# Kernel tuning notes

Hardware: AMD Instinct MI355X
Metric: run time of the kernel (lower is better)

Reference implementation:

```python
import jax, jax.numpy as jnp
import numpy as np

L, M, DIN, DEM, DH, GH, DOUT = 4, 4, 128, 64, 400, 256, 8
B = 16384
EPS = 1e-5


def setup_inputs() -> dict:
    key = jax.random.key(0)
    ks = iter(jax.random.split(key, 48))
    def p(shape, s=0.05):
        return jax.random.normal(next(ks), shape, jnp.float32) * s
    return dict(
        x=p((B, DIN), 1.0), embedding_input=p((B, DEM), 1.0),
        base_w1=p((DIN, DH)), base_b1=p((DH,)), base_w2=p((DH, DH)), base_b2=p((DH,)),
        em_w=p((DEM, DH)), em_b=p((DH,)),
        gfc_w1=p((DH, GH)), gfc_b1=p((GH,)), gfc_w2=p((GH, GH)), gfc_b2=p((GH,)),
        gw0_w=p((GH, M * M)), gw0_b=p((M * M,)),
        cond1_w=p((M * M, GH)), cond1_b=p((GH,)), gw1_w=p((GH, M * M)), gw1_b=p((M * M,)),
        cond2_w=p((2 * M * M, GH)), cond2_b=p((GH,)), gw2_w=p((GH, M * M)), gw2_b=p((M * M,)),
        condL_w=p((3 * M * M, GH)), condL_b=p((GH,)), gwL_w=p((GH, M)), gwL_b=p((M,)),
        bn1_g=1.0 + p((L, M, DH)), bn1_b=p((L, M, DH)),
        mod_W=p((L, M, DH, DH)), mod_b=p((L, M, DH)),
        bn2_g=1.0 + p((L, M, DH)), bn2_b=p((L, M, DH)),
        last_w=p((DH, DOUT)), last_b=p((DOUT,)),
    )


def _bn(h, g, b):
    # training-mode BatchNorm1d over batch axis; h:[B,M,D], g,b:[M,D]
    mu = h.mean(axis=0)
    var = ((h - mu) ** 2).mean(axis=0)  # biased variance, as torch BN
    return (h - mu) / jnp.sqrt(var + EPS) * g + b


def reference(x, embedding_input,
              base_w1, base_b1, base_w2, base_b2, em_w, em_b,
              gfc_w1, gfc_b1, gfc_w2, gfc_b2,
              gw0_w, gw0_b, cond1_w, cond1_b, gw1_w, gw1_b,
              cond2_w, cond2_b, gw2_w, gw2_b,
              condL_w, condL_b, gwL_w, gwL_b,
              bn1_g, bn1_b, mod_W, mod_b, bn2_g, bn2_b,
              last_w, last_b):
    relu = jax.nn.relu
    b = x.shape[0]
    # base MLP (last activation = identity)
    out = relu(x @ base_w1 + base_b1) @ base_w2 + base_b2          # [B,DH]
    # embedding MLP (single layer, identity last activation)
    emb = embedding_input @ em_w + em_b                            # [B,DH]
    emb = emb * out                                                # cond_ob
    out = relu(out)
    # gating trunk
    emb = relu(emb)
    emb = relu(emb @ gfc_w1 + gfc_b1)
    emb = emb @ gfc_w2 + gfc_b2                                    # [B,GH]
    # routing weight 0
    raw0 = relu(emb) @ gw0_w + gw0_b                               # [B,M*M]
    w0 = jax.nn.softmax(raw0.reshape(b, M, M), axis=-1)
    weights = [w0]
    flat = [w0.reshape(b, M * M)]
    # cascaded routing weights (num_layers-2 = 2 extra)
    for cw, cb, gw, gb in ((cond1_w, cond1_b, gw1_w, gw1_b),
                           (cond2_w, cond2_b, gw2_w, gw2_b)):
        cond = jnp.concatenate(flat, axis=-1) @ cw + cb            # [B,GH]
        cond = relu(cond * emb)
        w = jax.nn.softmax((cond @ gw + gb).reshape(b, M, M), axis=-1)
        weights.append(w)
        flat.append(w.reshape(b, M * M))
    # last (per-module) gating weight
    cond = jnp.concatenate(flat, axis=-1) @ condL_w + condL_b
    cond = relu(cond * emb)
    last_weight = jax.nn.softmax(cond @ gwL_w + gwL_b, axis=-1)    # [B,M]
    # module layer 0: all modules see the same input
    h = jnp.broadcast_to(out[:, None, :], (b, M, DH))
    h = _bn(h, bn1_g[0], bn1_b[0])
    mo = jnp.einsum('bmi,mio->bmo', h, mod_W[0]) + mod_b[0]
    mo = _bn(mo, bn2_g[0], bn2_b[0])                               # [B,M,DH]
    # cascaded module layers with soft routing
    for i in range(1, L):
        mi = relu(jnp.einsum('bkd,bjk->bjd', mo, weights[i - 1]))  # dispatch/combine
        h = _bn(mi, bn1_g[i], bn1_b[i])
        mo = jnp.einsum('bmi,mio->bmo', h, mod_W[i]) + mod_b[i]
        mo = _bn(mo, bn2_g[i], bn2_b[i])
    out = relu(jnp.einsum('bmd,bm->bd', mo, last_weight))
    return out @ last_w + last_b
```

## Files before the change

kernel.cpp:

```cpp
#include <hip/hip_runtime.h>
#include <hip/hip_bf16.h>

typedef __bf16 bf16_t;
typedef __bf16 bf16x8 __attribute__((ext_vector_type(8)));
typedef __bf16 bf16x4 __attribute__((ext_vector_type(4)));
typedef float  f32x4  __attribute__((ext_vector_type(4)));

#define BN_   16384
#define DIN_  128
#define DEM_  64
#define DH_   400
#define DHP_  416
#define DHA_  512
#define GH_   256
#define MM_   4
#define EPS_  1e-5f
#define PCOLS 448
#define NCH   128
#define NCHMI 512

__global__ __launch_bounds__(256) void k_detect(const unsigned* __restrict__ w,
                                                int* __restrict__ flag)
{
  __shared__ int cnt[256];
  int c = 0;
  for (int i = 0; i < 16; ++i) {
    unsigned v = w[threadIdx.x * 16 + i];
    float lo = __uint_as_float((v & 0xffffu) << 16);
    if (!(fabsf(lo) < 1e4f)) ++c;
  }
  cnt[threadIdx.x] = c;
  __syncthreads();
  if (threadIdx.x == 0) {
    int t = 0;
    for (int i = 0; i < 256; ++i) t += cnt[i];
    flag[0] = (t > 64) ? 1 : 0;
  }
}

__global__ void k_mfmaprobe(int* __restrict__ layC)
{
  int l = threadIdx.x & 63;
  bf16x8 av, bv;
#pragma unroll
  for (int e = 0; e < 8; ++e) { av[e] = (bf16_t)0.f; bv[e] = (bf16_t)0.f; }
  if ((l >> 4) == 0) av[0] = (bf16_t)(float)(l & 15);
  if (l == 0)        bv[0] = (bf16_t)1.f;
  f32x4 acc = {0.f, 0.f, 0.f, 0.f};
  acc = __builtin_amdgcn_mfma_f32_16x16x32_bf16(av, bv, acc, 0, 0, 0);
  if (l == 1) layC[0] = (acc[0] > 0.5f) ? 1 : 0;
}

__global__ __launch_bounds__(256) void k_convert(
    const void* __restrict__ src, bf16_t* __restrict__ dst, int n,
    const int* __restrict__ flag)
{
  const int f = flag[0];
  for (int i = blockIdx.x * 256 + threadIdx.x; i < n; i += gridDim.x * 256)
    dst[i] = f ? (bf16_t)((const float*)src)[i] : ((const bf16_t*)src)[i];
}

struct SmallTab {
  const void* src[26];
  bf16_t*     dst[26];
  int         n[26];
};

__global__ __launch_bounds__(256) void k_convert_smalls(SmallTab tab, const int* __restrict__ flag)
{
  const int f = flag[0];
  const void* s = tab.src[blockIdx.x];
  bf16_t*     d = tab.dst[blockIdx.x];
  const int   n = tab.n[blockIdx.x];
  for (int i = threadIdx.x; i < n; i += 256)
    d[i] = f ? (bf16_t)((const float*)s)[i] : ((const bf16_t*)s)[i];
}

template<bool SCALED>
__global__ __launch_bounds__(256) void k_transT(
    const void* __restrict__ src, size_t srcOff, size_t srcStride,
    bf16_t* __restrict__ dst, size_t dstStride,
    int K, int N, int KP, int NPa,
    const float* __restrict__ scale, const int* __restrict__ flag)
{
  __shared__ float T[64][65];
  const int f = flag ? flag[0] : 0;
  const int z = blockIdx.z;
  const float*  sf = (const float*) src + srcOff + (size_t)z * srcStride;
  const bf16_t* sb = (const bf16_t*)src + srcOff + (size_t)z * srcStride;
  bf16_t* dp = dst + (size_t)z * dstStride;
  const int k0 = blockIdx.x * 64, n0 = blockIdx.y * 64;
  const int lr = threadIdx.x >> 6, ln = threadIdx.x & 63;
#pragma unroll
  for (int p = 0; p < 16; ++p) {
    int kl = p * 4 + lr;
    int k = k0 + kl, n = n0 + ln;
    float v = 0.f;
    if (k < K && n < N)
      v = f ? sf[(size_t)k * N + n] : (float)sb[(size_t)k * N + n];
    if (SCALED && k < K) v *= scale[z * DHP_ + k];
    T[kl][ln] = v;
  }
  __syncthreads();
#pragma unroll
  for (int p = 0; p < 16; ++p) {
    int nl = p * 4 + lr;
    int n = n0 + nl, k = k0 + ln;
    if (n < NPa && k < KP) dp[(size_t)n * KP + k] = (bf16_t)T[ln][nl];
  }
}

__device__ __forceinline__ void gload_lds16(const bf16_t* g, bf16_t* l) {
#if __has_builtin(__builtin_amdgcn_global_load_lds)
  __builtin_amdgcn_global_load_lds((const __attribute__((address_space(1))) void*)g,
                                   (__attribute__((address_space(3))) void*)l, 16, 0, 0);
#else
  *(bf16x8*)l = *(const bf16x8*)g;
#endif
}

__device__ __forceinline__ void stage128x32(const bf16_t* __restrict__ g, int ld,
                                            bf16_t* lds, int t) {
  const int c1 = t + 256;
  const int q0 = ((t  & 3) ^ ((t  >> 3) & 3)) * 8;
  const int q1 = ((c1 & 3) ^ ((c1 >> 3) & 3)) * 8;
  gload_lds16(g + (size_t)(t  >> 2) * ld + q0, lds + t  * 8);
  gload_lds16(g + (size_t)(c1 >> 2) * ld + q1, lds + c1 * 8);
}

__device__ __forceinline__ void acc_zero(f32x4 (&acc)[4][4]) {
  const f32x4 z = {0.f, 0.f, 0.f, 0.f};
#pragma unroll
  for (int i = 0; i < 4; ++i)
#pragma unroll
    for (int j = 0; j < 4; ++j) acc[i][j] = z;
}

template<int KS>
__device__ __forceinline__ void gemm_staged(
    const bf16_t* __restrict__ ga, int lda,
    const bf16_t* __restrict__ gb, int ldb,
    bf16_t* ldsA, bf16_t* ldsB,
    int wr, int wc, int rr, int qq, int t,
    f32x4 (&acc)[4][4])
{
  const int qs = (qq ^ ((rr >> 1) & 3)) * 8;
  stage128x32(ga, lda, ldsA, t);
  stage128x32(gb, ldb, ldsB, t);
  int cur = 0;
#pragma unroll 1
  for (int ks = 0; ks < KS; ++ks) {
    __syncthreads();
    if (ks + 1 < KS) {
      stage128x32(ga + (ks + 1) * 32, lda, ldsA + (cur ^ 1) * 4096, t);
      stage128x32(gb + (ks + 1) * 32, ldb, ldsB + (cur ^ 1) * 4096, t);
    }
    const bf16_t* la = ldsA + cur * 4096;
    const bf16_t* lb = ldsB + cur * 4096;
    bf16x8 av[4], bv[4];
#pragma unroll
    for (int i = 0; i < 4; ++i)
      av[i] = *reinterpret_cast<const bf16x8*>(la + (wr + i * 16 + rr) * 32 + qs);
#pragma unroll
    for (int i = 0; i < 4; ++i)
      bv[i] = *reinterpret_cast<const bf16x8*>(lb + (wc + i * 16 + rr) * 32 + qs);
#pragma unroll
    for (int i = 0; i < 4; ++i)
#pragma unroll
      for (int j = 0; j < 4; ++j)
        acc[i][j] = __builtin_amdgcn_mfma_f32_16x16x32_bf16(av[i], bv[j], acc[i][j], 0, 0, 0);
    __syncthreads();
    cur ^= 1;
  }
}

template<int KS, bool RELU, bool OUTF32>
__global__ __launch_bounds__(256, 4) void k_gemm_bias(
    const bf16_t* __restrict__ A, int lda,
    const bf16_t* __restrict__ Bt, int ldb,
    const bf16_t* __restrict__ bias, int nbias,
    void* __restrict__ outv, int ldo, int nout,
    const int* __restrict__ layC)
{
  __shared__ bf16_t sAB[4 * 4096];
  const int lay = layC[0];
  const int t = threadIdx.x;
  const int w = t >> 6, lane = t & 63;
  const int rr = lane & 15, qq = lane >> 4;
  const int wr = (w >> 1) * 64, wc = (w & 1) * 64;
  const int rowT = blockIdx.x * 128, colT = blockIdx.y * 128;
  f32x4 acc[4][4]; acc_zero(acc);
// ... 194 lines not shown
  const int row0 = rowT + wr, col0 = colT + wc;
  float bjv[4];
  bool cok[4];
#pragma unroll
  for (int j = 0; j < 4; ++j) {
    int c = col0 + j * 16 + rr;
    bjv[j] = bM[m * DHA_ + c];
    cok[j] = (c < DHP_);
  }
  float s[4] = {0.f, 0.f, 0.f, 0.f}, q[4] = {0.f, 0.f, 0.f, 0.f};
  if (lay == 0) {
#pragma unroll
    for (int j = 0; j < 4; ++j) {
      if (!cok[j]) continue;
#pragma unroll
      for (int i = 0; i < 4; ++i)
#pragma unroll
        for (int e = 0; e < 4; ++e) {
          float v = acc[i][j][e] + bjv[j];
          s[j] += v; q[j] += v * v;
        }
    }
    bf16_t* eld = sAB + w * 2304;
#pragma unroll
    for (int p = 0; p < 2; ++p) {
#pragma unroll
      for (int ii = 0; ii < 2; ++ii) {
        int i = p * 2 + ii;
#pragma unroll
        for (int j = 0; j < 4; ++j)
#pragma unroll
          for (int e = 0; e < 4; ++e)
            eld[(ii * 16 + qq * 4 + e) * 72 + j * 16 + rr] = (bf16_t)(acc[i][j][e] + bjv[j]);
      }
#pragma unroll
      for (int rb = 0; rb < 4; ++rb) {
        int rl = rb * 8 + (lane >> 3);
        int c8 = (lane & 7) * 8;
        bf16x8 vv = *reinterpret_cast<const bf16x8*>(eld + rl * 72 + c8);
        int row = row0 + p * 32 + rl;
        int col = colT + wc + c8;
        if (col < DHP_)
          *reinterpret_cast<bf16x8*>(mo + ((size_t)row * MM_ + m) * DHP_ + col) = vv;
      }
    }
  } else {
#pragma unroll
    for (int j = 0; j < 4; ++j) {
#pragma unroll
      for (int i = 0; i < 4; ++i) {
#pragma unroll
        for (int e = 0; e < 4; ++e) {
          int row = row0 + i * 16 + rr;
          int col = col0 + j * 16 + qq * 4 + e;
          if (col >= DHP_) continue;
          float v = acc[i][j][e] + bM[m * DHA_ + col];
          mo[((size_t)row * MM_ + m) * DHP_ + col] = (bf16_t)v;
        }
      }
    }
  }
#pragma unroll
  for (int j = 0; j < 4; ++j) {
    s[j] += __shfl_xor(s[j], 16); s[j] += __shfl_xor(s[j], 32);
    q[j] += __shfl_xor(q[j], 16); q[j] += __shfl_xor(q[j], 32);
  }
  if (lane < 16) {
#pragma unroll
    for (int j = 0; j < 4; ++j) {
      rs[w >> 1][(w & 1) * 64 + j * 16 + lane] = s[j];
      rq[w >> 1][(w & 1) * 64 + j * 16 + lane] = q[j];
    }
  }
  __syncthreads();
  if (lay == 0 && t < 128) {
    int col = blockIdx.y * 128 + t;
    if (col < PCOLS) {
      ps[((size_t)blockIdx.x * MM_ + m) * PCOLS + col] = rs[0][t] + rs[1][t];
      pq[((size_t)blockIdx.x * MM_ + m) * PCOLS + col] = rq[0][t] + rq[1][t];
    }
  }
}

__global__ __launch_bounds__(256) void k_stats(
    const bf16_t* __restrict__ src, int nm,
    float* __restrict__ ps, float* __restrict__ pq,
    const int* __restrict__ layC)
{
  if (layC[0] == 0) return;
  __shared__ float lsum[4 * 52 * 8], lsq[4 * 52 * 8];
  const int m = blockIdx.x, ch = blockIdx.y;
  const int sub = threadIdx.x >> 6, lane = threadIdx.x & 63;
  float s[8], q[8];
#pragma unroll
  for (int e = 0; e < 8; ++e) { s[e] = 0.f; q[e] = 0.f; }
  if (lane < 52) {
    for (int i = 0; i < 32; ++i) {
      int b = ch * 128 + sub + i * 4;
      bf16x8 v = *reinterpret_cast<const bf16x8*>(src + ((size_t)b * nm + m) * DHP_ + lane * 8);
#pragma unroll
      for (int e = 0; e < 8; ++e) {
        float f = (float)v[e];
        s[e] += f; q[e] += f * f;
      }
    }
#pragma unroll
    for (int e = 0; e < 8; ++e) {
      lsum[(sub * 52 + lane) * 8 + e] = s[e];
      lsq [(sub * 52 + lane) * 8 + e] = q[e];
    }
  }
  __syncthreads();
  for (int idx = threadIdx.x; idx < 416; idx += 256) {
    float S = lsum[idx] + lsum[416 + idx] + lsum[832 + idx] + lsum[1248 + idx];
    float Q = lsq [idx] + lsq [416 + idx] + lsq [832 + idx] + lsq [1248 + idx];
    ps[((size_t)ch * MM_ + m) * PCOLS + idx] = S;
    pq[((size_t)ch * MM_ + m) * PCOLS + idx] = Q;
  }
}

template<int NCHT>
__global__ __launch_bounds__(512) void k_bnprep2(
    const float* __restrict__ ps, const float* __restrict__ pq, int per_m,
    const bf16_t* __restrict__ g, const bf16_t* __restrict__ b,
    float* __restrict__ s_o, float* __restrict__ t_o)
{
  __shared__ float lS[8][64], lQ[8][64];
  const int m = blockIdx.x, cg = blockIdx.y;
  const int sub = threadIdx.x >> 6, lane = threadIdx.x & 63;
  const int k = cg * 64 + lane;
  const int mm = per_m ? m : 0;
  float S = 0.f, Q = 0.f;
#pragma unroll 8
  for (int ch = sub; ch < NCHT; ch += 8) {
    size_t idx = ((size_t)ch * MM_ + mm) * PCOLS + k;
    S += ps[idx];
    Q += pq[idx];
  }
  lS[sub][lane] = S; lQ[sub][lane] = Q;
  __syncthreads();
  if (sub == 0 && k < DHP_) {
    float St = 0.f, Qt = 0.f;
#pragma unroll
    for (int i = 0; i < 8; ++i) { St += lS[i][lane]; Qt += lQ[i][lane]; }
    float s = 0.f, t = 0.f;
    if (k < DH_) {
      float mean = St * (1.f / BN_);
      float var  = fmaxf(Qt * (1.f / BN_) - mean * mean, 0.f);
      float rstd = rsqrtf(var + EPS_);
      s = (float)g[m * DH_ + k] * rstd;
      t = (float)b[m * DH_ + k] - mean * s;
    }
    s_o[m * DHP_ + k] = s;
    t_o[m * DHP_ + k] = t;
  }
}

__global__ __launch_bounds__(256) void k_foldB(
    const void* __restrict__ modW, size_t off, const bf16_t* __restrict__ modb,
    const float* __restrict__ t1v, float* __restrict__ bM,
    const int* __restrict__ flag)
{
  __shared__ float ls[256];
  const int f = flag[0];
  const int m = blockIdx.x, ncg = blockIdx.y;
  const int t = threadIdx.x;
  const int n = ncg * 64 + (t & 63);
  const int ks = t >> 6;
  float a = 0.f;
  if (n < DH_) {
    for (int k = ks * 100; k < ks * 100 + 100; ++k) {
      size_t idx = off + ((size_t)m * DH_ + k) * DH_ + n;
      float wv = f ? ((const float*)modW)[idx] : (float)((const bf16_t*)modW)[idx];
      a += t1v[m * DHP_ + k] * wv;
    }
  }
  ls[t] = a;
  __syncthreads();
  if (t < 64) {
    int nn = ncg * 64 + t;
    float v = ls[t] + ls[t + 64] + ls[t + 128] + ls[t + 192];
    if (nn < DH_) v += (float)modb[m * DH_ + nn];
    else v = 0.f;
    bM[m * DHA_ + nn] = v;
  }
  if (ncg == 6 && t < 64) bM[m * DHA_ + 448 + t] = 0.f;
}

__global__ __launch_bounds__(256) void k_mix(
    const bf16_t* __restrict__ mo, const float* __restrict__ s2v, const float* __restrict__ t2v,
    const float* __restrict__ wbuf, int woff, bf16_t* __restrict__ mi,
    float* __restrict__ ps, float* __restrict__ pq)
{
  __shared__ float sB[4 * 416], qB[4 * 416];
  const int ch = blockIdx.x;
  const int wave = threadIdx.x >> 6, lane = threadIdx.x & 63;
  const int d0 = lane * 8;
  float sx[4][8], tx[4][8];
  float sAcc[4][8], qAcc[4][8];
#pragma unroll
  for (int j = 0; j < 4; ++j)
#pragma unroll
    for (int e = 0; e < 8; ++e) { sAcc[j][e] = 0.f; qAcc[j][e] = 0.f; }
  if (lane < 52) {
#pragma unroll
    for (int k = 0; k < 4; ++k)
#pragma unroll
      for (int e = 0; e < 8; ++e) {
        sx[k][e] = s2v[k * DHP_ + d0 + e];
        tx[k][e] = t2v[k * DHP_ + d0 + e];
      }
  }
#pragma unroll 1
  for (int i = 0; i < 8; ++i) {
    int b = ch * 32 + wave + i * 4;
    float wv = (lane < 16) ? wbuf[(size_t)b * 52 + woff + lane] : 0.f;
    if (lane < 52) {
      float x[4][8];
#pragma unroll
      for (int k = 0; k < 4; ++k) {
        bf16x8 v = *reinterpret_cast<const bf16x8*>(mo + ((size_t)b * MM_ + k) * DHP_ + d0);
#pragma unroll
        for (int e = 0; e < 8; ++e)
          x[k][e] = (float)v[e] * sx[k][e] + tx[k][e];
      }
#pragma unroll
      for (int j = 0; j < 4; ++j) {
        float w0 = __shfl(wv, j * 4 + 0), w1 = __shfl(wv, j * 4 + 1);
        float w2 = __shfl(wv, j * 4 + 2), w3 = __shfl(wv, j * 4 + 3);
        bf16x8 ov;
#pragma unroll
        for (int e = 0; e < 8; ++e) {
          float a = fmaxf(x[0][e] * w0 + x[1][e] * w1 + x[2][e] * w2 + x[3][e] * w3, 0.f);
          ov[e] = (bf16_t)a;
          float r = (float)ov[e];
          sAcc[j][e] += r; qAcc[j][e] += r * r;
        }
        *reinterpret_cast<bf16x8*>(mi + ((size_t)b * MM_ + j) * DHP_ + d0) = ov;
      }
    }
  }
#pragma unroll 1
  for (int w = 0; w < 4; ++w) {
    if (wave == w && lane < 52) {
#pragma unroll
      for (int j = 0; j < 4; ++j)
#pragma unroll
        for (int e = 0; e < 8; ++e) {
          int idx = j * 416 + d0 + e;
          if (w == 0) { sB[idx] = sAcc[j][e]; qB[idx] = qAcc[j][e]; }
          else        { sB[idx] += sAcc[j][e]; qB[idx] += qAcc[j][e]; }
        }
    }
    __syncthreads();
  }
  for (int idx = threadIdx.x; idx < 4 * 416; idx += 256) {
    int j = idx / 416, col = idx - j * 416;
    ps[((size_t)ch * MM_ + j) * PCOLS + col] = sB[idx];
    pq[((size_t)ch * MM_ + j) * PCOLS + col] = qB[idx];
  }
}

__global__ __launch_bounds__(256) void k_gate(
    const bf16_t* __restrict__ emb,
    const bf16_t* __restrict__ gw0t, const bf16_t* __restrict__ gw0_b,
    const bf16_t* __restrict__ c1_w,  const bf16_t* __restrict__ c1_b,
    const bf16_t* __restrict__ gw1t, const bf16_t* __restrict__ gw1_b,
    const bf16_t* __restrict__ c2_w,  const bf16_t* __restrict__ c2_b,
    const bf16_t* __restrict__ gw2t, const bf16_t* __restrict__ gw2_b,
    const bf16_t* __restrict__ cL_w,  const bf16_t* __restrict__ cL_b,
    const bf16_t* __restrict__ gwLt, const bf16_t* __restrict__ gwL_b,
    float* __restrict__ wbuf)
{
  __shared__ float VBA[4][272], VBB[4][272];
  __shared__ float FLA[4][64], FLB[4][64];
  const int wave = threadIdx.x >> 6, lane = threadIdx.x & 63;
  float* vbA = VBA[wave];
  float* vbB = VBB[wave];
  float* flA = FLA[wave];
  float* flB = FLB[wave];
  const int bA = blockIdx.x * 8 + wave * 2, bB = bA + 1;
  const int wrIdx = lane * 4 + (lane >> 4) * 4;

  float eA[4], eB[4];
  {
    bf16x4 evA = *reinterpret_cast<const bf16x4*>(emb + (size_t)bA * GH_ + lane * 4);
    bf16x4 evB = *reinterpret_cast<const bf16x4*>(emb + (size_t)bB * GH_ + lane * 4);
    f32x4 rA, rB;
#pragma unroll
    for (int e = 0; e < 4; ++e) {
      eA[e] = (float)evA[e]; rA[e] = fmaxf(eA[e], 0.f);
      eB[e] = (float)evB[e]; rB[e] = fmaxf(eB[e], 0.f);
    }
    *reinterpret_cast<f32x4*>(vbA + wrIdx) = rA;
    *reinterpret_cast<f32x4*>(vbB + wrIdx) = rB;
  }
  __builtin_amdgcn_wave_barrier();

  const int hh = lane >> 4, jj = lane & 15;

  auto softmax4 = [&](float a) -> float {
    float m1 = fmaxf(a, __shfl_xor(a, 1));
    float mx = fmaxf(m1, __shfl_xor(m1, 2));
    float ex = __expf(a - mx);
    float sx = ex + __shfl_xor(ex, 1);
    float sm = sx + __shfl_xor(sx, 2);
    return ex / sm;
  };

  auto gw_phase = [&](const bf16_t* Wt, const bf16_t* Bb, int foff) {
    float a0A = 0.f, a1A = 0.f, a0B = 0.f, a1B = 0.f;
#pragma unroll
    for (int cc = 0; cc < 8; ++cc) {
      int c8 = (cc + hh * 2) & 7;
      int k  = hh * 64 + c8 * 8;
      int idx = k + hh * 4;
      f32x4 vA0 = *reinterpret_cast<const f32x4*>(vbA + idx);
      f32x4 vA1 = *reinterpret_cast<const f32x4*>(vbA + idx + 4);
      f32x4 vB0 = *reinterpret_cast<const f32x4*>(vbB + idx);
      f32x4 vB1 = *reinterpret_cast<const f32x4*>(vbB + idx + 4);
      bf16x8 wv = *reinterpret_cast<const bf16x8*>(Wt + jj * 256 + k);
      float w0 = (float)wv[0], w1 = (float)wv[1], w2 = (float)wv[2], w3 = (float)wv[3];
      float w4 = (float)wv[4], w5 = (float)wv[5], w6 = (float)wv[6], w7 = (float)wv[7];
      a0A = fmaf(vA0[0], w0, a0A); a0A = fmaf(vA0[1], w1, a0A);
      a0A = fmaf(vA0[2], w2, a0A); a0A = fmaf(vA0[3], w3, a0A);
      a1A = fmaf(vA1[0], w4, a1A); a1A = fmaf(vA1[1], w5, a1A);
      a1A = fmaf(vA1[2], w6, a1A); a1A = fmaf(vA1[3], w7, a1A);
      a0B = fmaf(vB0[0], w0, a0B); a0B = fmaf(vB0[1], w1, a0B);
      a0B = fmaf(vB0[2], w2, a0B); a0B = fmaf(vB0[3], w3, a0B);
      a1B = fmaf(vB1[0], w4, a1B); a1B = fmaf(vB1[1], w5, a1B);
      a1B = fmaf(vB1[2], w6, a1B); a1B = fmaf(vB1[3], w7, a1B);
    }
    float aA = a0A + a1A, aB = a0B + a1B;
    aA += __shfl_xor(aA, 16); aA += __shfl_xor(aA, 32);
    aB += __shfl_xor(aB, 16); aB += __shfl_xor(aB, 32);
    float bb = (float)Bb[jj];
    aA += bb; aB += bb;
    float wA = softmax4(aA), wB = softmax4(aB);
    if (lane < 16) {
      flA[foff + jj] = wA; wbuf[(size_t)bA * 52 + foff + jj] = wA;
      flB[foff + jj] = wB; wbuf[(size_t)bB * 52 + foff + jj] = wB;
    }
    __builtin_amdgcn_wave_barrier();
  };

  auto cond_phase = [&](const bf16_t* W, const bf16_t* Bb, int tcount) {
    float a4A[4], a4B[4];
    bf16x4 bb = *reinterpret_cast<const bf16x4*>(Bb + lane * 4);
#pragma unroll
    for (int e = 0; e < 4; ++e) { a4A[e] = (float)bb[e]; a4B[e] = a4A[e]; }
    for (int t = 0; t < tcount; ++t) {
      float fA = flA[t], fB = flB[t];
      bf16x4 wv = *reinterpret_cast<const bf16x4*>(W + t * 256 + lane * 4);
#pragma unroll
      for (int e = 0; e < 4; ++e) {
        float w = (float)wv[e];
        a4A[e] = fmaf(fA, w, a4A[e]);
        a4B[e] = fmaf(fB, w, a4B[e]);
      }
    }
    f32x4 rA, rB;
#pragma unroll
    for (int e = 0; e < 4; ++e) {
      rA[e] = fmaxf(a4A[e] * eA[e], 0.f);
      rB[e] = fmaxf(a4B[e] * eB[e], 0.f);
    }
    *reinterpret_cast<f32x4*>(vbA + wrIdx) = rA;
    *reinterpret_cast<f32x4*>(vbB + wrIdx) = rB;
    __builtin_amdgcn_wave_barrier();
  };

  gw_phase(gw0t, gw0_b, 0);
  cond_phase(c1_w, c1_b, 16);
  gw_phase(gw1t, gw1_b, 16);
  cond_phase(c2_w, c2_b, 32);
  gw_phase(gw2t, gw2_b, 32);
  cond_phase(cL_w, cL_b, 48);
  {
    const int j4 = lane & 3, h16 = lane >> 2;
    const int base = h16 * 16 + (h16 >> 2) * 4;
    bf16x8 w0 = *reinterpret_cast<const bf16x8*>(gwLt + j4 * 256 + h16 * 16);
    bf16x8 w1 = *reinterpret_cast<const bf16x8*>(gwLt + j4 * 256 + h16 * 16 + 8);
    float aA = 0.f, aB = 0.f;
#pragma unroll
    for (int c = 0; c < 2; ++c) {
      f32x4 vA0 = *reinterpret_cast<const f32x4*>(vbA + base + c * 8);
      f32x4 vA1 = *reinterpret_cast<const f32x4*>(vbA + base + c * 8 + 4);
      f32x4 vB0 = *reinterpret_cast<const f32x4*>(vbB + base + c * 8);
      f32x4 vB1 = *reinterpret_cast<const f32x4*>(vbB + base + c * 8 + 4);
      const bf16x8& w = c ? w1 : w0;
#pragma unroll
      for (int e = 0; e < 4; ++e) {
        aA = fmaf(vA0[e], (float)w[e], aA);
        aA = fmaf(vA1[e], (float)w[e + 4], aA);
        aB = fmaf(vB0[e], (float)w[e], aB);
        aB = fmaf(vB1[e], (float)w[e + 4], aB);
      }
    }
    aA += __shfl_xor(aA, 4); aA += __shfl_xor(aA, 8);
    aA += __shfl_xor(aA, 16); aA += __shfl_xor(aA, 32);
    aB += __shfl_xor(aB, 4); aB += __shfl_xor(aB, 8);
    aB += __shfl_xor(aB, 16); aB += __shfl_xor(aB, 32);
    float bb = (float)gwL_b[j4];
    aA += bb; aB += bb;
    float wA = softmax4(aA), wB = softmax4(aB);
    if (lane < 4) {
      wbuf[(size_t)bA * 52 + 48 + j4] = wA;
      wbuf[(size_t)bB * 52 + 48 + j4] = wB;
    }
  }
}

__global__ __launch_bounds__(256) void k_final(
    const bf16_t* __restrict__ mo, const float* __restrict__ s2v, const float* __restrict__ t2v,
    const float* __restrict__ wbuf, const bf16_t* __restrict__ last_w,
    const bf16_t* __restrict__ last_b, void* __restrict__ outv,
    const int* __restrict__ flag)
{
  const int f32out = flag[0];
  const int wave = threadIdx.x >> 6, lane = threadIdx.x & 63;
  const int d0 = lane * 8;
  float sx[4][8], tx[4][8];
  if (lane < 52) {
#pragma unroll
    for (int k = 0; k < 4; ++k)
#pragma unroll
      for (int e = 0; e < 8; ++e) {
        sx[k][e] = s2v[k * DHP_ + d0 + e];
        tx[k][e] = t2v[k * DHP_ + d0 + e];
      }
  }
  for (int b = blockIdx.x * 4 + wave; b < BN_; b += gridDim.x * 4) {
    const float* lwp = wbuf + (size_t)b * 52 + 48;
    float lm0 = lwp[0], lm1 = lwp[1], lm2 = lwp[2], lm3 = lwp[3];
    float slm = lm0 + lm1 + lm2 + lm3;
    const float* w0p = wbuf + (size_t)b * 52;
    float sw0 = w0p[0] + w0p[1] + w0p[2] + w0p[3];
    float p[8];
#pragma unroll
    for (int j = 0; j < 8; ++j) p[j] = 0.f;
    if (lane < 52) {
      float x[4][8];
#pragma unroll
      for (int k = 0; k < 4; ++k) {
        bf16x8 v = *reinterpret_cast<const bf16x8*>(mo + ((size_t)b * MM_ + k) * DHP_ + d0);
#pragma unroll
        for (int e = 0; e < 8; ++e)
          x[k][e] = (float)v[e] * sx[k][e] + tx[k][e];
      }
#pragma unroll
      for (int e = 0; e < 8; ++e) {
        float v = fmaxf(x[0][e] * lm0 + x[1][e] * lm1 + x[2][e] * lm2 + x[3][e] * lm3, 0.f);
        bf16x8 wv = *reinterpret_cast<const bf16x8*>(last_w + (size_t)(d0 + e) * 8);
#pragma unroll
        for (int j = 0; j < 8; ++j) p[j] = fmaf(v, (float)wv[j], p[j]);
      }
    }
#pragma unroll
    for (int j = 0; j < 8; ++j) {
      p[j] += __shfl_xor(p[j], 1);
      p[j] += __shfl_xor(p[j], 2);
      p[j] += __shfl_xor(p[j], 4);
      p[j] += __shfl_xor(p[j], 8);
      p[j] += __shfl_xor(p[j], 16);
      p[j] += __shfl_xor(p[j], 32);
    }
    float sel = p[0];
#pragma unroll
    for (int j = 1; j < 8; ++j) if (lane == j) sel = p[j];
    if (lane < 8) {
      float res = sel + (float)last_b[lane];
      if (!(fabsf(res) < 1e4f)) res = 400.f;
      if (!(slm > 0.97f && slm < 1.03f)) res = 1000.f;
      if (!(sw0 > 0.97f && sw0 < 1.03f)) res = 2000.f;
      if (f32out) ((float*)outv)[(size_t)b * 8 + lane] = res;
      else ((bf16_t*)outv)[(size_t)b * 8 + lane] = (bf16_t)res;
    }
  }
}

extern "C" void kernel_launch(void* const* d_in, const int* in_sizes, int n_in,
                              void* d_out, int out_size, void* d_ws, size_t ws_size,
                              hipStream_t stream)
{
  (void)in_sizes; (void)n_in;
  const void* x_raw   = d_in[0];
  const void* emb_raw = d_in[1];
  const void* base_w1 = d_in[2];
  const void* base_w2 = d_in[4];
  const void* em_w    = d_in[6];
  const void* gfc_w1  = d_in[8];
  const void* gfc_w2  = d_in[10];
  const void* modW_raw= d_in[28];

  char* base = (char*)d_ws;
  size_t off = 0;
  auto alloc = [&](size_t bytes) -> char* {
    off = (off + 255) & ~(size_t)255;
    char* r = base + off; off += bytes; return r;
  };
  int*    dflag = (int*)   alloc(16);
  int*    layC  = (int*)   alloc(16);
  bf16_t* Wt1  = (bf16_t*)alloc((size_t)512 * 128 * 2);
  bf16_t* Wem  = (bf16_t*)alloc((size_t)512 * 64 * 2);
  bf16_t* Wt2  = (bf16_t*)alloc((size_t)512 * DHP_ * 2);
  bf16_t* Wg1  = (bf16_t*)alloc((size_t)256 * DHP_ * 2);
  bf16_t* Wg2  = (bf16_t*)alloc((size_t)256 * 256 * 2);
  bf16_t* WtM  = (bf16_t*)alloc((size_t)MM_ * DHA_ * DHP_ * 2);
  float*  bM   = (float*) alloc((size_t)MM_ * DHA_ * 4);
  bf16_t* xc   = (bf16_t*)alloc((size_t)BN_ * DIN_ * 2);
  bf16_t* embc = (bf16_t*)alloc((size_t)BN_ * DEM_ * 2);
  bf16_t* out1 = (bf16_t*)alloc((size_t)BN_ * DHP_ * 2);
  bf16_t* emb0 = (bf16_t*)alloc((size_t)BN_ * DHP_ * 2);
  bf16_t* outA = (bf16_t*)alloc((size_t)BN_ * DHP_ * 2);
  bf16_t* emb1 = (bf16_t*)alloc((size_t)BN_ * DHP_ * 2);
  bf16_t* embF = (bf16_t*)alloc((size_t)BN_ * GH_ * 2);
  float*  wbuf = (float*) alloc((size_t)BN_ * 52 * 4);
  bf16_t* mo   = (bf16_t*)alloc((size_t)BN_ * MM_ * DHP_ * 2);
  bf16_t* mi   = (bf16_t*)alloc((size_t)BN_ * MM_ * DHP_ * 2);
  float* psO = (float*)alloc((size_t)NCH * MM_ * PCOLS * 4);
  float* pqO = (float*)alloc((size_t)NCH * MM_ * PCOLS * 4);
  float* psA = (float*)alloc((size_t)NCHMI * MM_ * PCOLS * 4);
  float* pqA = (float*)alloc((size_t)NCHMI * MM_ * PCOLS * 4);
  float* psB = (float*)alloc((size_t)NCH * MM_ * PCOLS * 4);
  float* pqB = (float*)alloc((size_t)NCH * MM_ * PCOLS * 4);
  float* s1 = (float*)alloc((size_t)MM_ * DHP_ * 4);
  float* t1 = (float*)alloc((size_t)MM_ * DHP_ * 4);
  float* s2 = (float*)alloc((size_t)MM_ * DHP_ * 4);
  float* t2 = (float*)alloc((size_t)MM_ * DHP_ * 4);
  bf16_t* gw0t = (bf16_t*)alloc((size_t)16 * 256 * 2);
  bf16_t* gw1t = (bf16_t*)alloc((size_t)16 * 256 * 2);
  bf16_t* gw2t = (bf16_t*)alloc((size_t)16 * 256 * 2);
  bf16_t* gwLt = (bf16_t*)alloc((size_t)4 * 256 * 2);
  const int NS = 26;
  const int sn[NS] = {400, 400, 400, 256, 256,
                      4096, 16, 4096, 256, 4096, 16, 8192, 256, 4096, 16,
                      12288, 256, 1024, 4,
                      6400, 6400, 6400, 6400, 6400, 3200, 8};
  const int si[NS] = {3, 5, 7, 9, 11,
                      12, 13, 14, 15, 16, 17, 18, 19, 20, 21,
                      22, 23, 24, 25,
                      26, 27, 29, 30, 31, 32, 33};
  bf16_t* sc[NS];
  for (int i = 0; i < NS; ++i) sc[i] = (bf16_t*)alloc((size_t)sn[i] * 2);
  bf16_t *b1c = sc[0], *b2c = sc[1], *embbc = sc[2], *g1bc = sc[3], *g2bc = sc[4];
  bf16_t *gw0w = sc[5], *gw0b = sc[6], *c1w = sc[7], *c1b = sc[8], *gw1w = sc[9],
         *gw1b = sc[10], *c2w = sc[11], *c2b = sc[12], *gw2w = sc[13], *gw2b = sc[14],
         *cLw = sc[15], *cLb = sc[16], *gwLw = sc[17], *gwLb = sc[18];
  bf16_t *bn1g = sc[19], *bn1b = sc[20], *modbc = sc[21], *bn2g = sc[22], *bn2b = sc[23];
  bf16_t *lastw = sc[24], *lastb = sc[25];

  if (off > ws_size) {
    hipMemsetAsync(d_out, 0, (size_t)out_size * 2, stream);
    return;
  }

  dim3 blk(256);
  k_detect<<<1, blk, 0, stream>>>((const unsigned*)x_raw, dflag);
  k_mfmaprobe<<<1, dim3(64), 0, stream>>>(layC);

  k_convert<<<dim3(2048), blk, 0, stream>>>(x_raw,   xc,    BN_ * DIN_, dflag);
  k_convert<<<dim3(1024), blk, 0, stream>>>(emb_raw, embc,  BN_ * DEM_, dflag);
  SmallTab tab;
  for (int i = 0; i < NS; ++i) { tab.src[i] = d_in[si[i]]; tab.dst[i] = sc[i]; tab.n[i] = sn[i]; }
  k_convert_smalls<<<dim3(NS), blk, 0, stream>>>(tab, dflag);

  k_transT<false><<<dim3(2, 8, 1), blk, 0, stream>>>(base_w1, 0, 0, Wt1, 0, DIN_, DH_, 128, 512, nullptr, dflag);
  k_transT<false><<<dim3(1, 8, 1), blk, 0, stream>>>(em_w,    0, 0, Wem, 0, DEM_, DH_, 64, 512, nullptr, dflag);
  k_transT<false><<<dim3(7, 8, 1), blk, 0, stream>>>(base_w2, 0, 0, Wt2, 0, DH_, DH_, DHP_, 512, nullptr, dflag);
  k_transT<false><<<dim3(7, 4, 1), blk, 0, stream>>>(gfc_w1,  0, 0, Wg1, 0, DH_, GH_, DHP_, GH_, nullptr, dflag);
  k_transT<false><<<dim3(4, 4, 1), blk, 0, stream>>>(gfc_w2,  0, 0, Wg2, 0, GH_, GH_, GH_, GH_, nullptr, dflag);
  k_transT<false><<<dim3(4, 1, 1), blk, 0, stream>>>(gw0w, 0, 0, gw0t, 0, 256, 16, 256, 16, nullptr, nullptr);
  k_transT<false><<<dim3(4, 1, 1), blk, 0, stream>>>(gw1w, 0, 0, gw1t, 0, 256, 16, 256, 16, nullptr, nullptr);
  k_transT<false><<<dim3(4, 1, 1), blk, 0, stream>>>(gw2w, 0, 0, gw2t, 0, 256, 16, 256, 16, nullptr, nullptr);
  k_transT<false><<<dim3(4, 1, 1), blk, 0, stream>>>(gwLw, 0, 0, gwLt, 0, 256, 4, 256, 4, nullptr, nullptr);

  k_gemm_bias<4,  true , false><<<dim3(128, 4), blk, 0, stream>>>(xc, DIN_, Wt1, 128, b1c, DH_, out1, DHP_, DHP_, layC);
  k_gemm_bias<2,  false, false><<<dim3(128, 4), blk, 0, stream>>>(embc, DEM_, Wem, 64, embbc, DH_, emb0, DHP_, DHP_, layC);
  k_gemm_base2<<<dim3(128, 4), blk, 0, stream>>>(out1, Wt2, b2c, emb0, outA, emb1, psO, pqO, layC);
  k_stats<<<dim3(1, NCH), blk, 0, stream>>>(outA, 1, psO, pqO, layC);
  bf16_t* emb2 = emb0;
  k_gemm_bias<13, true , false><<<dim3(128, 2), blk, 0, stream>>>(emb1, DHP_, Wg1, DHP_, g1bc, GH_, emb2, GH_, GH_, layC);
  k_gemm_bias<8,  false, false><<<dim3(128, 2), blk, 0, stream>>>(emb2, GH_, Wg2, GH_, g2bc, GH_, embF, GH_, GH_, layC);

  k_gate<<<dim3(BN_ / 8), blk, 0, stream>>>(embF,
      gw0t, gw0b, c1w, c1b, gw1t, gw1b, c2w, c2b, gw2t, gw2b,
      cLw, cLb, gwLt, gwLb, wbuf);

  k_bnprep2<NCH><<<dim3(4, 7), dim3(512), 0, stream>>>(psO, pqO, 0, bn1g, bn1b, s1, t1);
  k_transT<true><<<dim3(7, 8, 4), blk, 0, stream>>>(modW_raw, 0, (size_t)DH_ * DH_,
                                                    WtM, (size_t)DHA_ * DHP_, DH_, DH_, DHP_, DHA_, s1, dflag);
  k_foldB<<<dim3(4, 7), blk, 0, stream>>>(modW_raw, 0, modbc, t1, bM, dflag);
  k_gemm_mod<<<dim3(128, 4, 4), blk, 0, stream>>>(outA, DHP_, 0, WtM, bM, mo, psB, pqB, layC);
  k_stats<<<dim3(4, NCH), blk, 0, stream>>>(mo, MM_, psB, pqB, layC);

  for (int L = 1; L < 4; ++L) {
    k_bnprep2<NCH><<<dim3(4, 7), dim3(512), 0, stream>>>(psB, pqB, 1,
        bn2g + (size_t)(L - 1) * MM_ * DH_, bn2b + (size_t)(L - 1) * MM_ * DH_, s2, t2);
    k_mix<<<dim3(NCHMI), blk, 0, stream>>>(mo, s2, t2, wbuf, (L - 1) * 16, mi, psA, pqA);
    k_bnprep2<NCHMI><<<dim3(4, 7), dim3(512), 0, stream>>>(psA, pqA, 1,
        bn1g + (size_t)L * MM_ * DH_, bn1b + (size_t)L * MM_ * DH_, s1, t1);
    k_transT<true><<<dim3(7, 8, 4), blk, 0, stream>>>(modW_raw, (size_t)L * MM_ * DH_ * DH_, (size_t)DH_ * DH_,
                                                      WtM, (size_t)DHA_ * DHP_, DH_, DH_, DHP_, DHA_, s1, dflag);
    k_foldB<<<dim3(4, 7), blk, 0, stream>>>(modW_raw, (size_t)L * MM_ * DH_ * DH_, modbc + (size_t)L * MM_ * DH_, t1, bM, dflag);
    k_gemm_mod<<<dim3(128, 4, 4), blk, 0, stream>>>(mi, MM_ * DHP_, DHP_, WtM, bM, mo, psB, pqB, layC);
    k_stats<<<dim3(4, NCH), blk, 0, stream>>>(mo, MM_, psB, pqB, layC);
  }

  k_bnprep2<NCH><<<dim3(4, 7), dim3(512), 0, stream>>>(psB, pqB, 1,
      bn2g + (size_t)3 * MM_ * DH_, bn2b + (size_t)3 * MM_ * DH_, s2, t2);
  k_final<<<dim3(1024), blk, 0, stream>>>(mo, s2, t2, wbuf, lastw, lastb, d_out, dflag);
}
```

Before: 630.6 us.

## Drop fallback stats kernels, store gate weights as fp32, halve mix chunk count

```diff
diff --git a/kernel.cpp b/kernel.cpp
--- a/kernel.cpp
+++ b/kernel.cpp
@@ -17,7 +17,7 @@
 #define EPS_  1e-5f
 #define PCOLS 448
 #define NCH   128
-#define NCHMI 512
+#define NCHMI 256
 
 __global__ __launch_bounds__(256) void k_detect(const unsigned* __restrict__ w,
                                                 int* __restrict__ flag)
@@ -60,26 +60,34 @@
     dst[i] = f ? (bf16_t)((const float*)src)[i] : ((const bf16_t*)src)[i];
 }
 
+#define NS_ 29
 struct SmallTab {
-  const void* src[26];
-  bf16_t*     dst[26];
-  int         n[26];
+  const void* src[NS_];
+  void*       dst[NS_];
+  int         n[NS_];
+  int         of32[NS_];
 };
 
 __global__ __launch_bounds__(256) void k_convert_smalls(SmallTab tab, const int* __restrict__ flag)
 {
   const int f = flag[0];
   const void* s = tab.src[blockIdx.x];
-  bf16_t*     d = tab.dst[blockIdx.x];
   const int   n = tab.n[blockIdx.x];
-  for (int i = threadIdx.x; i < n; i += 256)
-    d[i] = f ? (bf16_t)((const float*)s)[i] : ((const bf16_t*)s)[i];
-}
-
-template<bool SCALED>
+  if (tab.of32[blockIdx.x]) {
+    float* d = (float*)tab.dst[blockIdx.x];
+    for (int i = threadIdx.x; i < n; i += 256)
+      d[i] = f ? ((const float*)s)[i] : (float)((const bf16_t*)s)[i];
+  } else {
+    bf16_t* d = (bf16_t*)tab.dst[blockIdx.x];
+    for (int i = threadIdx.x; i < n; i += 256)
+      d[i] = f ? (bf16_t)((const float*)s)[i] : ((const bf16_t*)s)[i];
+  }
+}
+
+template<bool SCALED, bool OUTF32>
 __global__ __launch_bounds__(256) void k_transT(
     const void* __restrict__ src, size_t srcOff, size_t srcStride,
-    bf16_t* __restrict__ dst, size_t dstStride,
+    void* __restrict__ dst, size_t dstStride,
     int K, int N, int KP, int NPa,
     const float* __restrict__ scale, const int* __restrict__ flag)
 {
@@ -88,7 +96,6 @@
   const int z = blockIdx.z;
   const float*  sf = (const float*) src + srcOff + (size_t)z * srcStride;
   const bf16_t* sb = (const bf16_t*)src + srcOff + (size_t)z * srcStride;
-  bf16_t* dp = dst + (size_t)z * dstStride;
   const int k0 = blockIdx.x * 64, n0 = blockIdx.y * 64;
   const int lr = threadIdx.x >> 6, ln = threadIdx.x & 63;
 #pragma unroll
@@ -106,7 +113,10 @@
   for (int p = 0; p < 16; ++p) {
     int nl = p * 4 + lr;
     int n = n0 + nl, k = k0 + ln;
-    if (n < NPa && k < KP) dp[(size_t)n * KP + k] = (bf16_t)T[ln][nl];
+    if (n < NPa && k < KP) {
+      if (OUTF32) ((float*)dst + (size_t)z * dstStride)[(size_t)n * KP + k] = T[ln][nl];
+      else ((bf16_t*)dst + (size_t)z * dstStride)[(size_t)n * KP + k] = (bf16_t)T[ln][nl];
+    }
   }
 }
 
@@ -467,43 +477,6 @@
   }
 }
 
-__global__ __launch_bounds__(256) void k_stats(
-    const bf16_t* __restrict__ src, int nm,
-    float* __restrict__ ps, float* __restrict__ pq,
-    const int* __restrict__ layC)
-{
-  if (layC[0] == 0) return;
-  __shared__ float lsum[4 * 52 * 8], lsq[4 * 52 * 8];
-  const int m = blockIdx.x, ch = blockIdx.y;
-  const int sub = threadIdx.x >> 6, lane = threadIdx.x & 63;
-  float s[8], q[8];
-#pragma unroll
-  for (int e = 0; e < 8; ++e) { s[e] = 0.f; q[e] = 0.f; }
-  if (lane < 52) {
-    for (int i = 0; i < 32; ++i) {
-      int b = ch * 128 + sub + i * 4;
-      bf16x8 v = *reinterpret_cast<const bf16x8*>(src + ((size_t)b * nm + m) * DHP_ + lane * 8);
-#pragma unroll
-      for (int e = 0; e < 8; ++e) {
-        float f = (float)v[e];
-        s[e] += f; q[e] += f * f;
-      }
-    }
-#pragma unroll
-    for (int e = 0; e < 8; ++e) {
-      lsum[(sub * 52 + lane) * 8 + e] = s[e];
-      lsq [(sub * 52 + lane) * 8 + e] = q[e];
-    }
-  }
-  __syncthreads();
-  for (int idx = threadIdx.x; idx < 416; idx += 256) {
-    float S = lsum[idx] + lsum[416 + idx] + lsum[832 + idx] + lsum[1248 + idx];
-    float Q = lsq [idx] + lsq [416 + idx] + lsq [832 + idx] + lsq [1248 + idx];
-    ps[((size_t)ch * MM_ + m) * PCOLS + idx] = S;
-    pq[((size_t)ch * MM_ + m) * PCOLS + idx] = Q;
-  }
-}
-
 template<int NCHT>
 __global__ __launch_bounds__(512) void k_bnprep2(
     const float* __restrict__ ps, const float* __restrict__ pq, int per_m,
@@ -597,8 +570,8 @@
       }
   }
 #pragma unroll 1
-  for (int i = 0; i < 8; ++i) {
-    int b = ch * 32 + wave + i * 4;
+  for (int i = 0; i < 16; ++i) {
+    int b = ch * 64 + wave + i * 4;
     float wv = (lane < 16) ? wbuf[(size_t)b * 52 + woff + lane] : 0.f;
     if (lane < 52) {
       float x[4][8];
@@ -648,13 +621,13 @@
 
 __global__ __launch_bounds__(256) void k_gate(
     const bf16_t* __restrict__ emb,
-    const bf16_t* __restrict__ gw0t, const bf16_t* __restrict__ gw0_b,
-    const bf16_t* __restrict__ c1_w,  const bf16_t* __restrict__ c1_b,
-    const bf16_t* __restrict__ gw1t, const bf16_t* __restrict__ gw1_b,
-    const bf16_t* __restrict__ c2_w,  const bf16_t* __restrict__ c2_b,
-    const bf16_t* __restrict__ gw2t, const bf16_t* __restrict__ gw2_b,
-    const bf16_t* __restrict__ cL_w,  const bf16_t* __restrict__ cL_b,
-    const bf16_t* __restrict__ gwLt, const bf16_t* __restrict__ gwL_b,
+    const float* __restrict__ gw0t, const bf16_t* __restrict__ gw0_b,
+    const float* __restrict__ c1f,  const bf16_t* __restrict__ c1_b,
+    const float* __restrict__ gw1t, const bf16_t* __restrict__ gw1_b,
+    const float* __restrict__ c2f,  const bf16_t* __restrict__ c2_b,
+    const float* __restrict__ gw2t, const bf16_t* __restrict__ gw2_b,
+    const float* __restrict__ cLf,  const bf16_t* __restrict__ cL_b,
+    const float* __restrict__ gwLt, const bf16_t* __restrict__ gwL_b,
     float* __restrict__ wbuf)
 {
   __shared__ float VBA[4][272], VBB[4][272];
@@ -693,7 +666,7 @@
     return ex / sm;
   };
 
-  auto gw_phase = [&](const bf16_t* Wt, const bf16_t* Bb, int foff) {
+  auto gw_phase = [&](const float* Wt, const bf16_t* Bb, int foff) {
     float a0A = 0.f, a1A = 0.f, a0B = 0.f, a1B = 0.f;
 #pragma unroll
     for (int cc = 0; cc < 8; ++cc) {
@@ -704,17 +677,16 @@
       f32x4 vA1 = *reinterpret_cast<const f32x4*>(vbA + idx + 4);
       f32x4 vB0 = *reinterpret_cast<const f32x4*>(vbB + idx);
       f32x4 vB1 = *reinterpret_cast<const f32x4*>(vbB + idx + 4);
-      bf16x8 wv = *reinterpret_cast<const bf16x8*>(Wt + jj * 256 + k);
-      float w0 = (float)wv[0], w1 = (float)wv[1], w2 = (float)wv[2], w3 = (float)wv[3];
-      float w4 = (float)wv[4], w5 = (float)wv[5], w6 = (float)wv[6], w7 = (float)wv[7];
-      a0A = fmaf(vA0[0], w0, a0A); a0A = fmaf(vA0[1], w1, a0A);
-      a0A = fmaf(vA0[2], w2, a0A); a0A = fmaf(vA0[3], w3, a0A);
-      a1A = fmaf(vA1[0], w4, a1A); a1A = fmaf(vA1[1], w5, a1A);
-      a1A = fmaf(vA1[2], w6, a1A); a1A = fmaf(vA1[3], w7, a1A);
-      a0B = fmaf(vB0[0], w0, a0B); a0B = fmaf(vB0[1], w1, a0B);
-      a0B = fmaf(vB0[2], w2, a0B); a0B = fmaf(vB0[3], w3, a0B);
-      a1B = fmaf(vB1[0], w4, a1B); a1B = fmaf(vB1[1], w5, a1B);
-      a1B = fmaf(vB1[2], w6, a1B); a1B = fmaf(vB1[3], w7, a1B);
+      f32x4 wv0 = *reinterpret_cast<const f32x4*>(Wt + jj * 256 + k);
+      f32x4 wv1 = *reinterpret_cast<const f32x4*>(Wt + jj * 256 + k + 4);
+      a0A = fmaf(vA0[0], wv0[0], a0A); a0A = fmaf(vA0[1], wv0[1], a0A);
+      a0A = fmaf(vA0[2], wv0[2], a0A); a0A = fmaf(vA0[3], wv0[3], a0A);
+      a1A = fmaf(vA1[0], wv1[0], a1A); a1A = fmaf(vA1[1], wv1[1], a1A);
+      a1A = fmaf(vA1[2], wv1[2], a1A); a1A = fmaf(vA1[3], wv1[3], a1A);
+      a0B = fmaf(vB0[0], wv0[0], a0B); a0B = fmaf(vB0[1], wv0[1], a0B);
+      a0B = fmaf(vB0[2], wv0[2], a0B); a0B = fmaf(vB0[3], wv0[3], a0B);
+      a1B = fmaf(vB1[0], wv1[0], a1B); a1B = fmaf(vB1[1], wv1[1], a1B);
+      a1B = fmaf(vB1[2], wv1[2], a1B); a1B = fmaf(vB1[3], wv1[3], a1B);
     }
     float aA = a0A + a1A, aB = a0B + a1B;
     aA += __shfl_xor(aA, 16); aA += __shfl_xor(aA, 32);
@@ -729,19 +701,18 @@
     __builtin_amdgcn_wave_barrier();
   };
 
-  auto cond_phase = [&](const bf16_t* W, const bf16_t* Bb, int tcount) {
+  auto cond_phase = [&](const float* W, const bf16_t* Bb, int tcount) {
     float a4A[4], a4B[4];
     bf16x4 bb = *reinterpret_cast<const bf16x4*>(Bb + lane * 4);
 #pragma unroll
     for (int e = 0; e < 4; ++e) { a4A[e] = (float)bb[e]; a4B[e] = a4A[e]; }
     for (int t = 0; t < tcount; ++t) {
       float fA = flA[t], fB = flB[t];
-      bf16x4 wv = *reinterpret_cast<const bf16x4*>(W + t * 256 + lane * 4);
+      f32x4 wv = *reinterpret_cast<const f32x4*>(W + t * 256 + lane * 4);
 #pragma unroll
       for (int e = 0; e < 4; ++e) {
-        float w = (float)wv[e];
-        a4A[e] = fmaf(fA, w, a4A[e]);
-        a4B[e] = fmaf(fB, w, a4B[e]);
+        a4A[e] = fmaf(fA, wv[e], a4A[e]);
+        a4B[e] = fmaf(fB, wv[e], a4B[e]);
       }
     }
     f32x4 rA, rB;
@@ -756,16 +727,14 @@
   };
 
   gw_phase(gw0t, gw0_b, 0);
-  cond_phase(c1_w, c1_b, 16);
+  cond_phase(c1f, c1_b, 16);
   gw_phase(gw1t, gw1_b, 16);
-  cond_phase(c2_w, c2_b, 32);
+  cond_phase(c2f, c2_b, 32);
   gw_phase(gw2t, gw2_b, 32);
-  cond_phase(cL_w, cL_b, 48);
+  cond_phase(cLf, cL_b, 48);
   {
     const int j4 = lane & 3, h16 = lane >> 2;
     const int base = h16 * 16 + (h16 >> 2) * 4;
-    bf16x8 w0 = *reinterpret_cast<const bf16x8*>(gwLt + j4 * 256 + h16 * 16);
-    bf16x8 w1 = *reinterpret_cast<const bf16x8*>(gwLt + j4 * 256 + h16 * 16 + 8);
     float aA = 0.f, aB = 0.f;
 #pragma unroll
     for (int c = 0; c < 2; ++c) {
@@ -773,13 +742,14 @@
       f32x4 vA1 = *reinterpret_cast<const f32x4*>(vbA + base + c * 8 + 4);
       f32x4 vB0 = *reinterpret_cast<const f32x4*>(vbB + base + c * 8);
       f32x4 vB1 = *reinterpret_cast<const f32x4*>(vbB + base + c * 8 + 4);
-      const bf16x8& w = c ? w1 : w0;
+      f32x4 w0 = *reinterpret_cast<const f32x4*>(gwLt + j4 * 256 + h16 * 16 + c * 8);
+      f32x4 w1 = *reinterpret_cast<const f32x4*>(gwLt + j4 * 256 + h16 * 16 + c * 8 + 4);
 #pragma unroll
       for (int e = 0; e < 4; ++e) {
-        aA = fmaf(vA0[e], (float)w[e], aA);
-        aA = fmaf(vA1[e], (float)w[e + 4], aA);
-        aB = fmaf(vB0[e], (float)w[e], aB);
-        aB = fmaf(vB1[e], (float)w[e + 4], aB);
+        aA = fmaf(vA0[e], w0[e], aA);
+        aA = fmaf(vA1[e], w1[e], aA);
+        aB = fmaf(vB0[e], w0[e], aB);
+        aB = fmaf(vB1[e], w1[e], aB);
       }
     }
     aA += __shfl_xor(aA, 4); aA += __shfl_xor(aA, 8);
@@ -913,25 +883,29 @@
   float* t1 = (float*)alloc((size_t)MM_ * DHP_ * 4);
   float* s2 = (float*)alloc((size_t)MM_ * DHP_ * 4);
   float* t2 = (float*)alloc((size_t)MM_ * DHP_ * 4);
-  bf16_t* gw0t = (bf16_t*)alloc((size_t)16 * 256 * 2);
-  bf16_t* gw1t = (bf16_t*)alloc((size_t)16 * 256 * 2);
-  bf16_t* gw2t = (bf16_t*)alloc((size_t)16 * 256 * 2);
-  bf16_t* gwLt = (bf16_t*)alloc((size_t)4 * 256 * 2);
-  const int NS = 26;
-  const int sn[NS] = {400, 400, 400, 256, 256,
-                      4096, 16, 4096, 256, 4096, 16, 8192, 256, 4096, 16,
-                      12288, 256, 1024, 4,
-                      6400, 6400, 6400, 6400, 6400, 3200, 8};
-  const int si[NS] = {3, 5, 7, 9, 11,
-                      12, 13, 14, 15, 16, 17, 18, 19, 20, 21,
-                      22, 23, 24, 25,
-                      26, 27, 29, 30, 31, 32, 33};
-  bf16_t* sc[NS];
-  for (int i = 0; i < NS; ++i) sc[i] = (bf16_t*)alloc((size_t)sn[i] * 2);
+  float* gw0t = (float*)alloc((size_t)16 * 256 * 4);
+  float* gw1t = (float*)alloc((size_t)16 * 256 * 4);
+  float* gw2t = (float*)alloc((size_t)16 * 256 * 4);
+  float* gwLt = (float*)alloc((size_t)4 * 256 * 4);
+  float* c1f  = (float*)alloc((size_t)16 * 256 * 4);
+  float* c2f  = (float*)alloc((size_t)32 * 256 * 4);
+  float* cLf  = (float*)alloc((size_t)48 * 256 * 4);
+  const int sn[NS_] = {400, 400, 400, 256, 256,
+                       4096, 16, 4096, 256, 4096, 16, 8192, 256, 4096, 16,
+                       12288, 256, 1024, 4,
+                       6400, 6400, 6400, 6400, 6400, 3200, 8,
+                       4096, 8192, 12288};
+  const int si[NS_] = {3, 5, 7, 9, 11,
+                       12, 13, 14, 15, 16, 17, 18, 19, 20, 21,
+                       22, 23, 24, 25,
+                       26, 27, 29, 30, 31, 32, 33,
+                       14, 18, 22};
+  bf16_t* sc[26];
+  for (int i = 0; i < 26; ++i) sc[i] = (bf16_t*)alloc((size_t)sn[i] * 2);
   bf16_t *b1c = sc[0], *b2c = sc[1], *embbc = sc[2], *g1bc = sc[3], *g2bc = sc[4];
-  bf16_t *gw0w = sc[5], *gw0b = sc[6], *c1w = sc[7], *c1b = sc[8], *gw1w = sc[9],
-         *gw1b = sc[10], *c2w = sc[11], *c2b = sc[12], *gw2w = sc[13], *gw2b = sc[14],
-         *cLw = sc[15], *cLb = sc[16], *gwLw = sc[17], *gwLb = sc[18];
+  bf16_t *gw0w = sc[5], *gw0b = sc[6], *c1b = sc[8], *gw1w = sc[9],
+         *gw1b = sc[10], *c2b = sc[12], *gw2w = sc[13], *gw2b = sc[14],
+         *cLb = sc[16], *gwLw = sc[17], *gwLb = sc[18];
   bf16_t *bn1g = sc[19], *bn1b = sc[20], *modbc = sc[21], *bn2g = sc[22], *bn2b = sc[23];
   bf16_t *lastw = sc[24], *lastb = sc[25];
 
@@ -947,37 +921,38 @@
   k_convert<<<dim3(2048), blk, 0, stream>>>(x_raw,   xc,    BN_ * DIN_, dflag);
   k_convert<<<dim3(1024), blk, 0, stream>>>(emb_raw, embc,  BN_ * DEM_, dflag);
   SmallTab tab;
-  for (int i = 0; i < NS; ++i) { tab.src[i] = d_in[si[i]]; tab.dst[i] = sc[i]; tab.n[i] = sn[i]; }
-  k_convert_smalls<<<dim3(NS), blk, 0, stream>>>(tab, dflag);
-
-  k_transT<false><<<dim3(2, 8, 1), blk, 0, stream>>>(base_w1, 0, 0, Wt1, 0, DIN_, DH_, 128, 512, nullptr, dflag);
-  k_transT<false><<<dim3(1, 8, 1), blk, 0, stream>>>(em_w,    0, 0, Wem, 0, DEM_, DH_, 64, 512, nullptr, dflag);
-  k_transT<false><<<dim3(7, 8, 1), blk, 0, stream>>>(base_w2, 0, 0, Wt2, 0, DH_, DH_, DHP_, 512, nullptr, dflag);
-  k_transT<false><<<dim3(7, 4, 1), blk, 0, stream>>>(gfc_w1,  0, 0, Wg1, 0, DH_, GH_, DHP_, GH_, nullptr, dflag);
-  k_transT<false><<<dim3(4, 4, 1), blk, 0, stream>>>(gfc_w2,  0, 0, Wg2, 0, GH_, GH_, GH_, GH_, nullptr, dflag);
-  k_transT<false><<<dim3(4, 1, 1), blk, 0, stream>>>(gw0w, 0, 0, gw0t, 0, 256, 16, 256, 16, nullptr, nullptr);
-  k_transT<false><<<dim3(4, 1, 1), blk, 0, stream>>>(gw1w, 0, 0, gw1t, 0, 256, 16, 256, 16, nullptr, nullptr);
-  k_transT<false><<<dim3(4, 1, 1), blk, 0, stream>>>(gw2w, 0, 0, gw2t, 0, 256, 16, 256, 16, nullptr, nullptr);
-  k_transT<false><<<dim3(4, 1, 1), blk, 0, stream>>>(gwLw, 0, 0, gwLt, 0, 256, 4, 256, 4, nullptr, nullptr);
+  for (int i = 0; i < 26; ++i) { tab.src[i] = d_in[si[i]]; tab.dst[i] = sc[i]; tab.n[i] = sn[i]; tab.of32[i] = 0; }
+  tab.src[26] = d_in[14]; tab.dst[26] = c1f; tab.n[26] = 4096;  tab.of32[26] = 1;
+  tab.src[27] = d_in[18]; tab.dst[27] = c2f; tab.n[27] = 8192;  tab.of32[27] = 1;
+  tab.src[28] = d_in[22]; tab.dst[28] = cLf; tab.n[28] = 12288; tab.of32[28] = 1;
+  k_convert_smalls<<<dim3(NS_), blk, 0, stream>>>(tab, dflag);
+
+  k_transT<false, false><<<dim3(2, 8, 1), blk, 0, stream>>>(base_w1, 0, 0, Wt1, 0, DIN_, DH_, 128, 512, nullptr, dflag);
+  k_transT<false, false><<<dim3(1, 8, 1), blk, 0, stream>>>(em_w,    0, 0, Wem, 0, DEM_, DH_, 64, 512, nullptr, dflag);
+  k_transT<false, false><<<dim3(7, 8, 1), blk, 0, stream>>>(base_w2, 0, 0, Wt2, 0, DH_, DH_, DHP_, 512, nullptr, dflag);
+  k_transT<false, false><<<dim3(7, 4, 1), blk, 0, stream>>>(gfc_w1,  0, 0, Wg1, 0, DH_, GH_, DHP_, GH_, nullptr, dflag);
+  k_transT<false, false><<<dim3(4, 4, 1), blk, 0, stream>>>(gfc_w2,  0, 0, Wg2, 0, GH_, GH_, GH_, GH_, nullptr, dflag);
+  k_transT<false, true><<<dim3(4, 1, 1), blk, 0, stream>>>(gw0w, 0, 0, gw0t, 0, 256, 16, 256, 16, nullptr, nullptr);
+  k_transT<false, true><<<dim3(4, 1, 1), blk, 0, stream>>>(gw1w, 0, 0, gw1t, 0, 256, 16, 256, 16, nullptr, nullptr);
+  k_transT<false, true><<<dim3(4, 1, 1), blk, 0, stream>>>(gw2w, 0, 0, gw2t, 0, 256, 16, 256, 16, nullptr, nullptr);
+  k_transT<false, true><<<dim3(4, 1, 1), blk, 0, stream>>>(gwLw, 0, 0, gwLt, 0, 256, 4, 256, 4, nullptr, nullptr);
 
   k_gemm_bias<4,  true , false><<<dim3(128, 4), blk, 0, stream>>>(xc, DIN_, Wt1, 128, b1c, DH_, out1, DHP_, DHP_, layC);
   k_gemm_bias<2,  false, false><<<dim3(128, 4), blk, 0, stream>>>(embc, DEM_, Wem, 64, embbc, DH_, emb0, DHP_, DHP_, layC);
   k_gemm_base2<<<dim3(128, 4), blk, 0, stream>>>(out1, Wt2, b2c, emb0, outA, emb1, psO, pqO, layC);
-  k_stats<<<dim3(1, NCH), blk, 0, stream>>>(outA, 1, psO, pqO, layC);
   bf16_t* emb2 = emb0;
   k_gemm_bias<13, true , false><<<dim3(128, 2), blk, 0, stream>>>(emb1, DHP_, Wg1, DHP_, g1bc, GH_, emb2, GH_, GH_, layC);
   k_gemm_bias<8,  false, false><<<dim3(128, 2), blk, 0, stream>>>(emb2, GH_, Wg2, GH_, g2bc, GH_, embF, GH_, GH_, layC);
 
   k_gate<<<dim3(BN_ / 8), blk, 0, stream>>>(embF,
-      gw0t, gw0b, c1w, c1b, gw1t, gw1b, c2w, c2b, gw2t, gw2b,
-      cLw, cLb, gwLt, gwLb, wbuf);
+      gw0t, gw0b, c1f, c1b, gw1t, gw1b, c2f, c2b, gw2t, gw2b,
+      cLf, cLb, gwLt, gwLb, wbuf);
 
   k_bnprep2<NCH><<<dim3(4, 7), dim3(512), 0, stream>>>(psO, pqO, 0, bn1g, bn1b, s1, t1);
-  k_transT<true><<<dim3(7, 8, 4), blk, 0, stream>>>(modW_raw, 0, (size_t)DH_ * DH_,
+  k_transT<true, false><<<dim3(7, 8, 4), blk, 0, stream>>>(modW_raw, 0, (size_t)DH_ * DH_,
                                                     WtM, (size_t)DHA_ * DHP_, DH_, DH_, DHP_, DHA_, s1, dflag);
   k_foldB<<<dim3(4, 7), blk, 0, stream>>>(modW_raw, 0, modbc, t1, bM, dflag);
   k_gemm_mod<<<dim3(128, 4, 4), blk, 0, stream>>>(outA, DHP_, 0, WtM, bM, mo, psB, pqB, layC);
-  k_stats<<<dim3(4, NCH), blk, 0, stream>>>(mo, MM_, psB, pqB, layC);
 
   for (int L = 1; L < 4; ++L) {
     k_bnprep2<NCH><<<dim3(4, 7), dim3(512), 0, stream>>>(psB, pqB, 1,
@@ -985,11 +960,10 @@
     k_mix<<<dim3(NCHMI), blk, 0, stream>>>(mo, s2, t2, wbuf, (L - 1) * 16, mi, psA, pqA);
     k_bnprep2<NCHMI><<<dim3(4, 7), dim3(512), 0, stream>>>(psA, pqA, 1,
         bn1g + (size_t)L * MM_ * DH_, bn1b + (size_t)L * MM_ * DH_, s1, t1);
-    k_transT<true><<<dim3(7, 8, 4), blk, 0, stream>>>(modW_raw, (size_t)L * MM_ * DH_ * DH_, (size_t)DH_ * DH_,
+    k_transT<true, false><<<dim3(7, 8, 4), blk, 0, stream>>>(modW_raw, (size_t)L * MM_ * DH_ * DH_, (size_t)DH_ * DH_,
                                                       WtM, (size_t)DHA_ * DHP_, DH_, DH_, DHP_, DHA_, s1, dflag);
     k_foldB<<<dim3(4, 7), blk, 0, stream>>>(modW_raw, (size_t)L * MM_ * DH_ * DH_, modbc + (size_t)L * MM_ * DH_, t1, bM, dflag);
     k_gemm_mod<<<dim3(128, 4, 4), blk, 0, stream>>>(mi, MM_ * DHP_, DHP_, WtM, bM, mo, psB, pqB, layC);
-    k_stats<<<dim3(4, NCH), blk, 0, stream>>>(mo, MM_, psB, pqB, layC);
   }
 
   k_bnprep2<NCH><<<dim3(4, 7), dim3(512), 0, stream>>>(psB, pqB, 1,
```

Result: no change. 640.2 us (+1.5%).
